# Kernel tuning notes

Measured on AMD Instinct MI355X. Metric: run time of the kernel, lower is better.

## Reference

```python
import jax, jax.numpy as jnp
import numpy as np

GRID_NUM = 28
IMG_SIZE = 224.0
GRID_SIZE = IMG_SIZE / GRID_NUM
LAMBDA_COORD = 5.0
LAMBDA_NOOBJ = 0.5
NUM_CLASSES = 20
EPS = 1e-12


def setup_inputs() -> dict:
    key = jax.random.key(0)
    k1, k2, k3 = jax.random.split(key, 3)
    B, S = 1024, GRID_NUM
    y_pred = jax.random.uniform(k1, (B, S, S, 30), dtype=jnp.float32)
    # y_true channel 0: class id in {0..20}; 0 means no object. channels 1:5: (x, y, w, h)
    cls = jax.random.randint(k2, (B, S, S, 1), 0, NUM_CLASSES + 1).astype(jnp.float32)
    box = jax.random.uniform(k3, (B, S, S, 4), dtype=jnp.float32)
    y_true = jnp.concatenate([cls, box], axis=-1)
    return {"y_pred": y_pred, "y_true": y_true}


def _corners(box, gi, gj):
    # box[..., 0:2] are cell-relative center offsets, box[..., 2:4] are image-relative w/h
    cx = (gj + box[..., 0]) * GRID_SIZE
    cy = (gi + box[..., 1]) * GRID_SIZE
    w = box[..., 2] * IMG_SIZE
    h = box[..., 3] * IMG_SIZE
    return cx - w / 2, cy - h / 2, cx + w / 2, cy + h / 2


def _iou(box_a, box_b, gi, gj):
    ax1, ay1, ax2, ay2 = _corners(box_a, gi, gj)
    bx1, by1, bx2, by2 = _corners(box_b, gi, gj)
    iw = jnp.maximum(jnp.minimum(ax2, bx2) - jnp.maximum(ax1, bx1), 0.0)
    ih = jnp.maximum(jnp.minimum(ay2, by2) - jnp.maximum(ay1, by1), 0.0)
    inter = iw * ih
    area_a = jnp.maximum(ax2 - ax1, 0.0) * jnp.maximum(ay2 - ay1, 0.0)
    area_b = jnp.maximum(bx2 - bx1, 0.0) * jnp.maximum(by2 - by1, 0.0)
    return inter / (area_a + area_b - inter + EPS)


def reference(y_pred, y_true):
    B, S = y_pred.shape[0], y_pred.shape[1]
    gi = jnp.arange(S, dtype=jnp.float32)[None, :, None]  # broadcast over (B, S, S)
    gj = jnp.arange(S, dtype=jnp.float32)[None, None, :]

    obj_mask = y_true[..., 0] != 0.0  # (B, S, S)
    true_box = y_true[..., 1:5]

    iou0 = _iou(y_pred[..., 0:4], true_box, gi, gj)
    iou1 = _iou(y_pred[..., 5:9], true_box, gi, gj)
    # original: choose 0 iff iou0 > iou1, else 1
    choose1 = ~(iou0 > iou1)

    conf_pred = jnp.where(choose1, y_pred[..., 9], y_pred[..., 4])
    conf_true = jnp.where(choose1, iou1, iou0)
    xy_pred = jnp.where(choose1[..., None], y_pred[..., 5:7], y_pred[..., 0:2])

    loss_conf_obj = jnp.square(conf_pred - conf_true)
    loss_coord = LAMBDA_COORD * jnp.sum(jnp.square(xy_pred - y_true[..., 1:3]), axis=-1)

    cls_idx = y_true[..., 0].astype(jnp.int32) - 1
    cls_onehot = jax.nn.one_hot(cls_idx, NUM_CLASSES, dtype=y_pred.dtype)
    loss_cls = jnp.sum(jnp.square(y_pred[..., 10:] - cls_onehot), axis=-1)

    loss_conf_noobj = LAMBDA_NOOBJ * (jnp.square(y_pred[..., 4]) + jnp.square(y_pred[..., 9]))

    bsz = jnp.float32(B)
    loss_confidence = jnp.sum(jnp.where(obj_mask, loss_conf_obj, loss_conf_noobj)) / bsz
    loss_coordinate = jnp.sum(jnp.where(obj_mask, loss_coord, 0.0)) / bsz
    loss_classification = jnp.sum(jnp.where(obj_mask, loss_cls, 0.0)) / bsz
    return loss_confidence + loss_coordinate + loss_classification
```

## Files before the change

### kernel.cpp

```cpp
#include <hip/hip_runtime.h>


#define S_GRID 28
#define N_CELLS (1024 * S_GRID * S_GRID)
#define CPB 128
#define NBLOCKS (N_CELLS / CPB)

typedef const __attribute__((address_space(1))) unsigned int* gptr_t;
typedef __attribute__((address_space(3))) unsigned int* lptr_t;

__device__ __forceinline__ float iou_calc(float bx, float by, float bw, float bh,
                                          float tx, float ty, float tw, float th,
                                          float gi, float gj) {
    float acx = (gj + bx) * 8.0f;
    float acy = (gi + by) * 8.0f;
    float aw  = bw * 224.0f;
    float ah  = bh * 224.0f;
    float ax1 = acx - aw * 0.5f, ax2 = acx + aw * 0.5f;
    float ay1 = acy - ah * 0.5f, ay2 = acy + ah * 0.5f;
    float bcx = (gj + tx) * 8.0f;
    float bcy = (gi + ty) * 8.0f;
    float btw = tw * 224.0f;
    float bth = th * 224.0f;
    float bx1 = bcx - btw * 0.5f, bx2 = bcx + btw * 0.5f;
    float by1 = bcy - bth * 0.5f, by2 = bcy + bth * 0.5f;

    float iw = fmaxf(fminf(ax2, bx2) - fmaxf(ax1, bx1), 0.0f);
    float ih = fmaxf(fminf(ay2, by2) - fmaxf(ay1, by1), 0.0f);
    float inter = iw * ih;
    float area_a = fmaxf(ax2 - ax1, 0.0f) * fmaxf(ay2 - ay1, 0.0f);
    float area_b = fmaxf(bx2 - bx1, 0.0f) * fmaxf(by2 - by1, 0.0f);
    return inter / (area_a + area_b - inter + 1e-12f);
}

__global__ __launch_bounds__(128) void yolo_loss_kernel(const float4* __restrict__ yp4,
                                                        const float4* __restrict__ yt4,
                                                        float* __restrict__ partials) {
    __shared__ float sp[CPB * 30];
    __shared__ __align__(16) float st[CPB * 5];
    __shared__ float wsum[2];

    int tid  = threadIdx.x;
    int lane = tid & 63;
    int wave = tid >> 6;

    const float4* pb = yp4 + (size_t)blockIdx.x * (CPB * 30 / 4);
#pragma unroll
    for (int k = 0; k < 8; ++k) {
        int c = k * 2 + wave;
        if (c < 15) {
            const float4* src = pb + c * 64 + lane;
            __builtin_amdgcn_global_load_lds((gptr_t)src,
                                             (lptr_t)(sp + c * 256),
                                             16, 0, 0);
        }
    }

    const float4* tb = yt4 + (size_t)blockIdx.x * (CPB * 5 / 4);
    float4 v0 = tb[tid];
    float4 v1 = (tid < 32) ? tb[128 + tid] : make_float4(0, 0, 0, 0);
    ((float4*)st)[tid] = v0;
    if (tid < 32) ((float4*)st)[128 + tid] = v1;

    __syncthreads();

    int c = blockIdx.x * CPB + tid;
    int ij = c % (S_GRID * S_GRID);
    float gi = (float)(ij / S_GRID);
    float gj = (float)(ij % S_GRID);

    float pr[30];
    const float* p = sp + tid * 30;
#pragma unroll
    for (int k = 0; k < 30; ++k) pr[k] = p[k];

    float tc = st[tid * 5 + 0];
    float tx = st[tid * 5 + 1];
    float ty = st[tid * 5 + 2];
    float tw = st[tid * 5 + 3];
    float th = st[tid * 5 + 4];

    float iou0 = iou_calc(pr[0], pr[1], pr[2], pr[3], tx, ty, tw, th, gi, gj);
    float iou1 = iou_calc(pr[5], pr[6], pr[7], pr[8], tx, ty, tw, th, gi, gj);
    bool choose1 = !(iou0 > iou1);

    float conf_pred = choose1 ? pr[9] : pr[4];
    float conf_true = choose1 ? iou1 : iou0;
    float xp = choose1 ? pr[5] : pr[0];
    float yp = choose1 ? pr[6] : pr[1];

    float dcf = conf_pred - conf_true;
    float d0 = xp - tx, d1 = yp - ty;

    int cls = (int)tc - 1;
    float lcls = 0.0f;
#pragma unroll
    for (int k = 0; k < 20; ++k) {
        float oh = (k == cls) ? 1.0f : 0.0f;
        float d = pr[10 + k] - oh;
        lcls += d * d;
    }

    float obj_loss   = dcf * dcf + 5.0f * (d0 * d0 + d1 * d1) + lcls;
    float noobj_loss = 0.5f * (pr[4] * pr[4] + pr[9] * pr[9]);
    float val = (tc != 0.0f) ? obj_loss : noobj_loss;

#pragma unroll
    for (int off = 32; off > 0; off >>= 1) {
        val += __shfl_down(val, off, 64);
    }
    if (lane == 0) wsum[wave] = val;
    __syncthreads();
    if (tid == 0) {
        partials[blockIdx.x] = wsum[0] + wsum[1];
    }
}

__global__ __launch_bounds__(256) void reduce_kernel(const float* __restrict__ partials,
                                                     float* __restrict__ out) {
    int tid = threadIdx.x;
    float s = 0.0f;
#pragma unroll
    for (int k = 0; k < 25; ++k) {
        int i = k * 256 + tid;
        if (i < NBLOCKS) s += partials[i];
    }
#pragma unroll
    for (int off = 32; off > 0; off >>= 1) {
        s += __shfl_down(s, off, 64);
    }
    __shared__ float wsum[4];
    int lane = tid & 63;
    int wid  = tid >> 6;
    if (lane == 0) wsum[wid] = s;
    __syncthreads();
    if (tid == 0) {
        out[0] = (wsum[0] + wsum[1] + wsum[2] + wsum[3]) * (1.0f / 1024.0f);
    }
}

extern "C" void kernel_launch(void* const* d_in, const int* in_sizes, int n_in,
                              void* d_out, int out_size, void* d_ws, size_t ws_size,
                              hipStream_t stream) {
    const float4* y_pred = (const float4*)d_in[0];
    const float4* y_true = (const float4*)d_in[1];
    float* out = (float*)d_out;
    float* partials = (float*)d_ws;

    yolo_loss_kernel<<<NBLOCKS, CPB, 0, stream>>>(y_pred, y_true, partials);
    reduce_kernel<<<1, 256, 0, stream>>>(partials, out);
}
```

Baseline: 153.1 us.

## Make each wave independent with register-staged loads and per-wave partials

Each wave now stages its own 64 cells of predictions through registers into a private LDS slice using float2 loads, replacing the async global_load_lds path and the block-wide barriers. Truth values are read directly from global memory per lane instead of being staged through LDS. Each wave writes its own partial sum, so the reduce kernel now sums 12544 partials instead of 6272. The aim is to remove __syncthreads stalls and let waves proceed independently, at the cost of narrower loads, strided truth reads and a larger final reduction.

Result: no change. 151.1 us (-1.3%).

```diff
diff --git a/kernel.cpp b/kernel.cpp
--- a/kernel.cpp
+++ b/kernel.cpp
@@ -3,11 +3,11 @@
 
 #define S_GRID 28
 #define N_CELLS (1024 * S_GRID * S_GRID)
-#define CPB 128
-#define NBLOCKS (N_CELLS / CPB)
-
-typedef const __attribute__((address_space(1))) unsigned int* gptr_t;
-typedef __attribute__((address_space(3))) unsigned int* lptr_t;
+#define CPW 64
+#define WPB 4
+#define BLOCK (WPB * 64)
+#define N_WAVES (N_CELLS / CPW)
+#define NBLOCKS (N_WAVES / WPB)
 
 __device__ __forceinline__ float iou_calc(float bx, float by, float bw, float bh,
                                           float tx, float ty, float tw, float th,
@@ -33,52 +33,37 @@
     return inter / (area_a + area_b - inter + 1e-12f);
 }
 
-__global__ __launch_bounds__(128) void yolo_loss_kernel(const float4* __restrict__ yp4,
-                                                        const float4* __restrict__ yt4,
-                                                        float* __restrict__ partials) {
-    __shared__ float sp[CPB * 30];
-    __shared__ __align__(16) float st[CPB * 5];
-    __shared__ float wsum[2];
+__global__ __launch_bounds__(BLOCK, 4) void yolo_loss_kernel(const float2* __restrict__ yp2,
+                                                             const float* __restrict__ yt,
+                                                             float* __restrict__ partials) {
+    __shared__ float sp[WPB][CPW * 30];
 
     int tid  = threadIdx.x;
     int lane = tid & 63;
     int wave = tid >> 6;
+    int gwave = blockIdx.x * WPB + wave;
 
-    const float4* pb = yp4 + (size_t)blockIdx.x * (CPB * 30 / 4);
+    const float2* pb = yp2 + (size_t)gwave * (CPW * 30 / 2);
+    float2 v[15];
 #pragma unroll
-    for (int k = 0; k < 8; ++k) {
-        int c = k * 2 + wave;
-        if (c < 15) {
-            const float4* src = pb + c * 64 + lane;
-            __builtin_amdgcn_global_load_lds((gptr_t)src,
-                                             (lptr_t)(sp + c * 256),
-                                             16, 0, 0);
-        }
-    }
+    for (int k = 0; k < 15; ++k) v[k] = pb[k * 64 + lane];
 
-    const float4* tb = yt4 + (size_t)blockIdx.x * (CPB * 5 / 4);
-    float4 v0 = tb[tid];
-    float4 v1 = (tid < 32) ? tb[128 + tid] : make_float4(0, 0, 0, 0);
-    ((float4*)st)[tid] = v0;
-    if (tid < 32) ((float4*)st)[128 + tid] = v1;
+    float2* spw2 = (float2*)sp[wave];
+#pragma unroll
+    for (int k = 0; k < 15; ++k) spw2[k * 64 + lane] = v[k];
 
-    __syncthreads();
-
-    int c = blockIdx.x * CPB + tid;
-    int ij = c % (S_GRID * S_GRID);
-    float gi = (float)(ij / S_GRID);
-    float gj = (float)(ij % S_GRID);
+    int cell = gwave * CPW + lane;
+    const float* t = yt + (size_t)cell * 5;
+    float tc = t[0], tx = t[1], ty = t[2], tw = t[3], th = t[4];
 
     float pr[30];
-    const float* p = sp + tid * 30;
+    const float* p = sp[wave] + lane * 30;
 #pragma unroll
     for (int k = 0; k < 30; ++k) pr[k] = p[k];
 
-    float tc = st[tid * 5 + 0];
-    float tx = st[tid * 5 + 1];
-    float ty = st[tid * 5 + 2];
-    float tw = st[tid * 5 + 3];
-    float th = st[tid * 5 + 4];
+    int ij = cell % (S_GRID * S_GRID);
+    float gi = (float)(ij / S_GRID);
+    float gj = (float)(ij % S_GRID);
 
     float iou0 = iou_calc(pr[0], pr[1], pr[2], pr[3], tx, ty, tw, th, gi, gj);
     float iou1 = iou_calc(pr[5], pr[6], pr[7], pr[8], tx, ty, tw, th, gi, gj);
@@ -109,11 +94,7 @@
     for (int off = 32; off > 0; off >>= 1) {
         val += __shfl_down(val, off, 64);
     }
-    if (lane == 0) wsum[wave] = val;
-    __syncthreads();
-    if (tid == 0) {
-        partials[blockIdx.x] = wsum[0] + wsum[1];
-    }
+    if (lane == 0) partials[gwave] = val;
 }
 
 __global__ __launch_bounds__(256) void reduce_kernel(const float* __restrict__ partials,
@@ -121,9 +102,8 @@
     int tid = threadIdx.x;
     float s = 0.0f;
 #pragma unroll
-    for (int k = 0; k < 25; ++k) {
-        int i = k * 256 + tid;
-        if (i < NBLOCKS) s += partials[i];
+    for (int k = 0; k < 49; ++k) {
+        s += partials[k * 256 + tid];
     }
 #pragma unroll
     for (int off = 32; off > 0; off >>= 1) {
@@ -142,11 +122,11 @@
 extern "C" void kernel_launch(void* const* d_in, const int* in_sizes, int n_in,
                               void* d_out, int out_size, void* d_ws, size_t ws_size,
                               hipStream_t stream) {
-    const float4* y_pred = (const float4*)d_in[0];
-    const float4* y_true = (const float4*)d_in[1];
+    const float2* y_pred = (const float2*)d_in[0];
+    const float*  y_true = (const float*)d_in[1];
     float* out = (float*)d_out;
     float* partials = (float*)d_ws;
 
-    yolo_loss_kernel<<<NBLOCKS, CPB, 0, stream>>>(y_pred, y_true, partials);
+    yolo_loss_kernel<<<NBLOCKS, BLOCK, 0, stream>>>(y_pred, y_true, partials);
     reduce_kernel<<<1, 256, 0, stream>>>(partials, out);
 }
```
